# Kernel optimization log

Measured on AMD Instinct MI355X. Metric: run time of the kernel, lower is better.

## Reference

```python
import jax, jax.numpy as jnp
import numpy as np

D_MODEL = 2048
HQ = 32          # query heads
HKV = 8          # kv heads
HD = D_MODEL // HQ   # head_dim = 64
G = HQ // HKV        # group size = 4
THETA = 10000.0


def _rope(x, pos):
    """x: (B, H, T, D), pos: (B, T) int. Rotates even/odd interleaved pairs."""
    D = x.shape[-1]
    inv_freq = THETA ** (-jnp.arange(0, D, 2, dtype=jnp.float32) / D)   # (D/2,)
    ang = pos[:, None, :, None].astype(jnp.float32) * inv_freq          # (B,1,T,D/2)
    cos, sin = jnp.cos(ang), jnp.sin(ang)
    x1, x2 = x[..., 0::2], x[..., 1::2]
    r1 = x1 * cos - x2 * sin
    r2 = x1 * sin + x2 * cos
    return jnp.stack([r1, r2], axis=-1).reshape(x.shape)


def setup_inputs() -> dict:
    key = jax.random.key(0)
    ks = jax.random.split(key, 5)
    B, T = 2, 2048
    s = lambda fan_in: 1.0 / np.sqrt(fan_in)
    return {
        "x": jax.random.normal(ks[0], (B, T, D_MODEL), jnp.float32),
        "token_positions": jnp.arange(T, dtype=jnp.int32),
        "WQ": jax.random.normal(ks[1], (HQ * HD, D_MODEL), jnp.float32) * s(D_MODEL),
        "WK": jax.random.normal(ks[2], (HKV * HD, D_MODEL), jnp.float32) * s(D_MODEL),
        "WV": jax.random.normal(ks[3], (HKV * HD, D_MODEL), jnp.float32) * s(D_MODEL),
        "WO": jax.random.normal(ks[4], (D_MODEL, HQ * HD), jnp.float32) * s(HQ * HD),
    }


def reference(x, token_positions, WQ, WK, WV, WO):
    B, T, _ = x.shape
    pos = token_positions if token_positions.ndim == 2 else jnp.broadcast_to(token_positions[None, :], (B, T))

    # Projections (Linear is y = x @ W.T, no bias)
    Q = (x @ WQ.T).reshape(B, T, HQ, HD).transpose(0, 2, 1, 3)    # (B,Hq,T,D)
    K = (x @ WK.T).reshape(B, T, HKV, HD).transpose(0, 2, 1, 3)   # (B,Hkv,T,D)
    V = (x @ WV.T).reshape(B, T, HKV, HD).transpose(0, 2, 1, 3)

    Q = _rope(Q, pos)
    K = _rope(K, pos)

    # GQA: group query heads per kv head instead of duplicating K/V
    Qg = Q.reshape(B, HKV, G, T, HD)
    scale = jnp.float32(1.0 / np.sqrt(HD))
    scores = jnp.einsum('bkgqd,bkld->bkgql', Qg, K) * scale       # (B,Hkv,G,T,T)

    causal = jnp.tril(jnp.ones((T, T), dtype=bool))
    scores = jnp.where(causal, scores, jnp.finfo(scores.dtype).min)
    A = jax.nn.softmax(scores, axis=-1)

    O = jnp.einsum('bkgql,bkld->bkgqd', A, V)                     # (B,Hkv,G,T,D)
    O = O.reshape(B, HQ, T, HD).transpose(0, 2, 1, 3).reshape(B, T, HQ * HD)
    return O @ WO.T
```

## Files before the change

### kernel.cpp

```cpp
#include <hip/hip_runtime.h>
#include <hip/hip_bf16.h>

#define B_   2
#define T_   2048
#define DM_  2048
#define HQ_  32
#define HKV_ 8
#define HD_  64

typedef __attribute__((ext_vector_type(8))) short bf16x8;
typedef __attribute__((ext_vector_type(4))) float f32x4;
typedef __fp16 f16x4 __attribute__((ext_vector_type(4)));
typedef __fp16 f16x2 __attribute__((ext_vector_type(2)));

__device__ __forceinline__ unsigned short f2bf(float f) {
    unsigned int u = __float_as_uint(f);
    u = (u + 0x7fffu + ((u >> 16) & 1u)) >> 16;
    return (unsigned short)u;
}

__device__ __forceinline__ void gload16(const unsigned short* g, unsigned short* l) {
    __builtin_amdgcn_global_load_lds(
        (const __attribute__((address_space(1))) unsigned int*)g,
        (__attribute__((address_space(3))) unsigned int*)l, 16, 0, 0);
}


__global__ __launch_bounds__(256) void convert_all(
    const float* __restrict__ x,  const float* __restrict__ WQ,
    const float* __restrict__ WK, const float* __restrict__ WV,
    const float* __restrict__ WO, unsigned short* __restrict__ ws)
{
    int i = blockIdx.x*256 + threadIdx.x;
    const float* src; unsigned short* dst; int rel;
    if (i < 2097152)      { src = x;  dst = ws;                 rel = i; }
    else if (i < 3145728) { src = WQ; dst = ws + 8388608;       rel = i - 2097152; }
    else if (i < 3407872) { src = WK; dst = ws + 8388608+4194304; rel = i - 3145728; }
    else if (i < 3670016) { src = WV; dst = ws + 8388608+5242880; rel = i - 3407872; }
    else                  { src = WO; dst = ws + 14680064;      rel = i - 3670016; }
    float4 v = *(const float4*)(src + (size_t)rel*4);
    uint2 pk;
    pk.x = (unsigned int)f2bf(v.x) | ((unsigned int)f2bf(v.y) << 16);
    pk.y = (unsigned int)f2bf(v.z) | ((unsigned int)f2bf(v.w) << 16);
    *(uint2*)(dst + (size_t)rel*4) = pk;
}

__global__ __launch_bounds__(256) void qkv_gemm_bf16(
    const unsigned short* __restrict__ Ab, const unsigned short* __restrict__ Wb,
    unsigned short* __restrict__ Qb, unsigned short* __restrict__ Kb,
    unsigned short* __restrict__ Vt)
{
    __shared__ unsigned short As[128*32];
    __shared__ unsigned short Bs[128*32];
    const int tid  = threadIdx.x;
    const int ln   = tid & 63;
    const int wv   = tid >> 6;
    const int wm   = (wv >> 1) * 64;
    const int wn   = (wv & 1) * 64;
    const int col  = ln & 15;
    const int quad = ln >> 4;
    const int m0   = blockIdx.y * 128;
    const int n0   = blockIdx.x * 128;

    const unsigned short* aG = Ab + (size_t)(m0 + (tid>>2))*DM_ + (tid&3)*8;
    const unsigned short* bG = Wb + (size_t)(n0 + (tid>>2))*DM_ + (tid&3)*8;
    unsigned short* aL0 = &As[wv*512];
    unsigned short* aL1 = &As[wv*512 + 2048];
    unsigned short* bL0 = &Bs[wv*512];
    unsigned short* bL1 = &Bs[wv*512 + 2048];

    f32x4 acc[4][4];
    #pragma unroll
    for (int i=0;i<4;++i)
        #pragma unroll
        for (int j=0;j<4;++j) { acc[i][j][0]=0.f; acc[i][j][1]=0.f; acc[i][j][2]=0.f; acc[i][j][3]=0.f; }

    for (int k0 = 0; k0 < DM_; k0 += 32) {
        __syncthreads();
        gload16(aG + k0,                  aL0);
        gload16(aG + (size_t)64*DM_ + k0, aL1);
        gload16(bG + k0,                  bL0);
        gload16(bG + (size_t)64*DM_ + k0, bL1);
        __syncthreads();
        bf16x8 af[4], bfr[4];
        #pragma unroll
        for (int i=0;i<4;++i) {
            af[i]  = *(const bf16x8*)&As[(wm + i*16 + col)*32 + quad*8];
            bfr[i] = *(const bf16x8*)&Bs[(wn + i*16 + col)*32 + quad*8];
        }
        #pragma unroll
        for (int i=0;i<4;++i)
            #pragma unroll
            for (int j=0;j<4;++j)
                acc[i][j] = __builtin_amdgcn_mfma_f32_16x16x32_bf16(af[i], bfr[j], acc[i][j], 0, 0, 0);
    }

    const int b  = m0 >> 11;
    const int tb = m0 & 2047;
    #pragma unroll
    for (int j=0;j<4;++j) {
        const int n = n0 + wn + j*16 + col;
        #pragma unroll
        for (int i=0;i<4;++i) {
            const int t = tb + wm + i*16 + quad*4;
            if (n < 2048) {
                #pragma unroll
                for (int r=0;r<4;++r)
                    Qb[(((size_t)(b*HQ_ + (n>>6)))*T_ + t + r)*HD_ + (n&63)] = f2bf(acc[i][j][r]);
            } else if (n < 2560) {
                #pragma unroll
                for (int r=0;r<4;++r)
                    Kb[(((size_t)(b*HKV_ + ((n-2048)>>6)))*T_ + t + r)*HD_ + (n&63)] = f2bf(acc[i][j][r]);
            } else {
                unsigned short* vp = Vt + (((size_t)(b*HKV_ + ((n-2560)>>6)))*HD_ + (n&63))*T_ + t;
                union { f16x2 h; unsigned int u; } c0, c1;
                c0.h = __builtin_amdgcn_cvt_pkrtz(acc[i][j][0], acc[i][j][1]);
                c1.h = __builtin_amdgcn_cvt_pkrtz(acc[i][j][2], acc[i][j][3]);
                *(unsigned int*)(vp)     = c0.u;
                *(unsigned int*)(vp + 2) = c1.u;
            }
        }
    }
}

__global__ __launch_bounds__(256) void rope_inplace(
    unsigned short* __restrict__ Qb, unsigned short* __restrict__ Kb,
    const int* __restrict__ pos)
{
    const int NQ = B_*HQ_*T_*(HD_/2);
    const int NK = B_*HKV_*T_*(HD_/2);
    int idx = blockIdx.x*256 + threadIdx.x;
    unsigned short* base; float scale;
    int rem;
    if (idx < NQ) { base = Qb; rem = idx; scale = 0.18033688011112042f; }
    else { rem = idx - NQ; if (rem >= NK) return; base = Kb; scale = 1.0f; }
    const int i  = rem & 31;
    const int t  = (rem >> 5) & (T_ - 1);
    const int bh = rem >> 16;
    size_t off = (((size_t)bh)*T_ + t)*HD_ + (i<<1);
    unsigned int pk = *(unsigned int*)(base + off);
    float x1 = __uint_as_float((pk & 0xffffu) << 16);
    float x2 = __uint_as_float(pk & 0xffff0000u);
    float p = (float)pos[t];
    float inv = exp2f(-13.287712379549449f * ((float)(i<<1)) * (1.0f/64.0f));
    float ang = p * inv;
    float sn, cs;
    sincosf(ang, &sn, &cs);
    float r1 = (x1*cs - x2*sn) * scale;
    float r2 = (x1*sn + x2*cs) * scale;
    unsigned int out = (unsigned int)f2bf(r1) | ((unsigned int)f2bf(r2) << 16);
    *(unsigned int*)(base + off) = out;
}

__global__ __launch_bounds__(256, 2) void attn_mfma(
    const unsigned short* __restrict__ Qb, const unsigned short* __restrict__ Kb,
    const unsigned short* __restrict__ Vh, unsigned short* __restrict__ Ob)
{
    __shared__ unsigned short Ks[2][64*64];
    __shared__ unsigned short Vs[2][64*64];

    const int tid  = threadIdx.x;
    const int lane = tid & 63;
    const int wave = tid >> 6;
    const int q16  = lane & 15;
    const int quad = lane >> 4;
    const int bxi  = blockIdx.x;
    const int bh   = blockIdx.y;
    const int b    = bh >> 5;
    const int h    = bh & 31;
    const int kvh  = h >> 2;
    const int qa   = bxi;
    const int qbt  = 31 - bxi;
    const int qgA  = qa *64 + wave*16 + q16;
    const int qgB  = qbt*64 + wave*16 + q16;

    const unsigned short* kbase = Kb + ((size_t)(b*HKV_ + kvh))*T_*HD_;
    const unsigned short* vbase = Vh + ((size_t)(b*HKV_ + kvh))*(size_t)HD_*T_;

    const bf16x8 qA0 = *(const bf16x8*)(Qb + ((size_t)bh*T_ + qgA)*HD_ + quad*8);
    const bf16x8 qA1 = *(const bf16x8*)(Qb + ((size_t)bh*T_ + qgA)*HD_ + 32 + quad*8);
    const bf16x8 qB0 = *(const bf16x8*)(Qb + ((size_t)bh*T_ + qgB)*HD_ + quad*8);
    const bf16x8 qB1 = *(const bf16x8*)(Qb + ((size_t)bh*T_ + qgB)*HD_ + 32 + quad*8);

    f32x4 oA[4], oB[4];
    #pragma unroll
    for (int i=0;i<4;++i) {
        oA[i][0]=0.f; oA[i][1]=0.f; oA[i][2]=0.f; oA[i][3]=0.f;
        oB[i][0]=0.f; oB[i][1]=0.f; oB[i][2]=0.f; oB[i][3]=0.f;
    }
    float lA = 0.f, lB = 0.f;

    const int sr = tid >> 3;
    const int sj = tid & 7;
    const int sc = (sj ^ (sr & 7)) * 8;

    const int rk7 = q16 & 7;
    const int ck0 = (quad ^ rk7) * 8;
    const int ck1 = ((quad + 4) ^ rk7) * 8;

    auto smrow = [&](const f32x4 s, float& ps) -> f16x4 {
        float e0 = exp2f(s[0]), e1 = exp2f(s[1]);
        float e2 = exp2f(s[2]), e3 = exp2f(s[3]);
        ps += (e0+e1) + (e2+e3);
        union { f16x2 h[2]; f16x4 v; } c;
        c.h[0] = __builtin_amdgcn_cvt_pkrtz(e0, e1);
        c.h[1] = __builtin_amdgcn_cvt_pkrtz(e2, e3);
        return c.v;
    };

    uint4 kr0, kr1, vr0, vr1;
    kr0 = *(const uint4*)(kbase + (size_t)sr*HD_ + sj*8);
    kr1 = *(const uint4*)(kbase + (size_t)(sr+32)*HD_ + sj*8);
    vr0 = *(const uint4*)(vbase + (size_t)sr*T_ + sj*8);
    vr1 = *(const uint4*)(vbase + (size_t)(sr+32)*T_ + sj*8);
    *(uint4*)&Ks[0][sr*64 + sc]      = kr0;
    *(uint4*)&Ks[0][(sr+32)*64 + sc] = kr1;
    *(uint4*)&Vs[0][sr*64 + sc]      = vr0;
    *(uint4*)&Vs[0][(sr+32)*64 + sc] = vr1;
    kr0 = *(const uint4*)(kbase + (size_t)(64+sr)*HD_ + sj*8);
    kr1 = *(const uint4*)(kbase + (size_t)(64+sr+32)*HD_ + sj*8);
    vr0 = *(const uint4*)(vbase + (size_t)sr*T_ + 64 + sj*8);
    vr1 = *(const uint4*)(vbase + (size_t)(sr+32)*T_ + 64 + sj*8);
    __syncthreads();

    int cur = 0;

    for (int kt = 0; kt <= qa; ++kt) {
        const unsigned short* KsC = Ks[cur];
        const unsigned short* VsC = Vs[cur];
        const int nxt = cur ^ 1;

        f32x4 sB[4], sA[4];
        #pragma unroll
        for (int t=0;t<4;++t) {
            sB[t][0]=0.f; sB[t][1]=0.f; sB[t][2]=0.f; sB[t][3]=0.f;
            sA[t][0]=0.f; sA[t][1]=0.f; sA[t][2]=0.f; sA[t][3]=0.f;
        }
        f16x4 pfB[4];
        float psB = 0.f, psA = 0.f;

        __builtin_amdgcn_s_setprio(1);
        #pragma unroll
        for (int t = 0; t < 4; ++t) {
            const int rk = (t*16 + q16) * 64;
            bf16x8 a0 = *(const bf16x8*)&KsC[rk + ck0];
            bf16x8 a1 = *(const bf16x8*)&KsC[rk + ck1];
            sB[t] = __builtin_amdgcn_mfma_f32_16x16x32_bf16(a0, qB0, sB[t], 0, 0, 0);
            sB[t] = __builtin_amdgcn_mfma_f32_16x16x32_bf16(a1, qB1, sB[t], 0, 0, 0);
            sA[t] = __builtin_amdgcn_mfma_f32_16x16x32_bf16(a0, qA0, sA[t], 0, 0, 0);
            sA[t] = __builtin_amdgcn_mfma_f32_16x16x32_bf16(a1, qA1, sA[t], 0, 0, 0);
            if (t > 0) pfB[t-1] = smrow(sB[t-1], psB);
        }
        *(uint4*)&Ks[nxt][sr*64 + sc]      = kr0;
        *(uint4*)&Ks[nxt][(sr+32)*64 + sc] = kr1;
        *(uint4*)&Vs[nxt][sr*64 + sc]      = vr0;
        *(uint4*)&Vs[nxt][(sr+32)*64 + sc] = vr1;
        if (kt + 1 < qbt) {
            const int kn = (kt+2)*64;
            kr0 = *(const uint4*)(kbase + (size_t)(kn+sr)*HD_ + sj*8);
            kr1 = *(const uint4*)(kbase + (size_t)(kn+sr+32)*HD_ + sj*8);
            vr0 = *(const uint4*)(vbase + (size_t)sr*T_ + kn + sj*8);
            vr1 = *(const uint4*)(vbase + (size_t)(sr+32)*T_ + kn + sj*8);
        }
        pfB[3] = smrow(sB[3], psB);
        lB += psB;

        if (kt == qa) {
            #pragma unroll
            for (int t = 0; t < 4; ++t)
                #pragma unroll
                for (int r = 0; r < 4; ++r)
                    if (kt*64 + t*16 + quad*4 + r > qgA) sA[t][r] = -1e30f;
        }

        #pragma unroll
        for (int t = 0; t < 4; ++t) {
            const int cv = ((2*t + (quad>>1)) ^ rk7) * 8 + (quad&1)*4;
            f16x4 va[4];
            #pragma unroll
            for (int dt=0;dt<4;++dt)
                va[dt] = *(const f16x4*)&VsC[(dt*16 + q16)*64 + cv];
            #pragma unroll
            for (int dt=0;dt<4;++dt)
                oB[dt] = __builtin_amdgcn_mfma_f32_16x16x16f16(va[dt], pfB[t], oB[dt], 0, 0, 0);
            f16x4 pfA = smrow(sA[t], psA);
            #pragma unroll
            for (int dt=0;dt<4;++dt)
                oA[dt] = __builtin_amdgcn_mfma_f32_16x16x16f16(va[dt], pfA, oA[dt], 0, 0, 0);
        }
        lA += psA;
        __builtin_amdgcn_s_setprio(0);
        __syncthreads();
        cur ^= 1;
    }

    for (int kt = qa+1; kt <= qbt; ++kt) {
        const unsigned short* KsC = Ks[cur];
        const unsigned short* VsC = Vs[cur];
        const int nxt = cur ^ 1;

        f32x4 sB[4];
        #pragma unroll
        for (int t=0;t<4;++t) { sB[t][0]=0.f; sB[t][1]=0.f; sB[t][2]=0.f; sB[t][3]=0.f; }

        __builtin_amdgcn_s_setprio(1);
        #pragma unroll
        for (int t = 0; t < 4; ++t) {
            const int rk = (t*16 + q16) * 64;
            bf16x8 a0 = *(const bf16x8*)&KsC[rk + ck0];
            bf16x8 a1 = *(const bf16x8*)&KsC[rk + ck1];
            sB[t] = __builtin_amdgcn_mfma_f32_16x16x32_bf16(a0, qB0, sB[t], 0, 0, 0);
            sB[t] = __builtin_amdgcn_mfma_f32_16x16x32_bf16(a1, qB1, sB[t], 0, 0, 0);
        }
        if (kt < qbt) {
            *(uint4*)&Ks[nxt][sr*64 + sc]      = kr0;
            *(uint4*)&Ks[nxt][(sr+32)*64 + sc] = kr1;
            *(uint4*)&Vs[nxt][sr*64 + sc]      = vr0;
            *(uint4*)&Vs[nxt][(sr+32)*64 + sc] = vr1;
        }
        if (kt + 1 < qbt) {
            const int kn = (kt+2)*64;
            kr0 = *(const uint4*)(kbase + (size_t)(kn+sr)*HD_ + sj*8);
            kr1 = *(const uint4*)(kbase + (size_t)(kn+sr+32)*HD_ + sj*8);
            vr0 = *(const uint4*)(vbase + (size_t)sr*T_ + kn + sj*8);
            vr1 = *(const uint4*)(vbase + (size_t)(sr+32)*T_ + kn + sj*8);
        }
        if (kt == qbt) {
            #pragma unroll
            for (int t = 0; t < 4; ++t)
                #pragma unroll
                for (int r = 0; r < 4; ++r)
                    if (kt*64 + t*16 + quad*4 + r > qgB) sB[t][r] = -1e30f;
        }

        float psB = 0.f;
        #pragma unroll
        for (int t = 0; t < 4; ++t) {
            f16x4 pfB = smrow(sB[t], psB);
            const int cv = ((2*t + (quad>>1)) ^ rk7) * 8 + (quad&1)*4;
            #pragma unroll
            for (int dt=0;dt<4;++dt) {
                f16x4 va = *(const f16x4*)&VsC[(dt*16 + q16)*64 + cv];
                oB[dt] = __builtin_amdgcn_mfma_f32_16x16x16f16(va, pfB, oB[dt], 0, 0, 0);
            }
        }
        lB += psB;
        __builtin_amdgcn_s_setprio(0);
        __syncthreads();
        cur ^= 1;
    }

    lA += __shfl_xor(lA, 16); lA += __shfl_xor(lA, 32);
    lB += __shfl_xor(lB, 16); lB += __shfl_xor(lB, 32);
    const float rlA = 1.0f / lA;
    const float rlB = 1.0f / lB;
    unsigned short* opA = Ob + ((size_t)(b*T_ + qgA))*(HQ_*HD_) + h*HD_;
    unsigned short* opB = Ob + ((size_t)(b*T_ + qgB))*(HQ_*HD_) + h*HD_;
    #pragma unroll
    for (int dt = 0; dt < 4; ++dt) {
        uint2 pa, pb;
        pa.x = (unsigned int)f2bf(oA[dt][0]*rlA) | ((unsigned int)f2bf(oA[dt][1]*rlA) << 16);
        pa.y = (unsigned int)f2bf(oA[dt][2]*rlA) | ((unsigned int)f2bf(oA[dt][3]*rlA) << 16);
        pb.x = (unsigned int)f2bf(oB[dt][0]*rlB) | ((unsigned int)f2bf(oB[dt][1]*rlB) << 16);
        pb.y = (unsigned int)f2bf(oB[dt][2]*rlB) | ((unsigned int)f2bf(oB[dt][3]*rlB) << 16);
        *(uint2*)(opA + dt*16 + quad*4) = pa;
        *(uint2*)(opB + dt*16 + quad*4) = pb;
    }
}

__global__ __launch_bounds__(256) void out_gemm_bf16(
    const unsigned short* __restrict__ Ab, const unsigned short* __restrict__ Wb,
    float* __restrict__ C)
{
    __shared__ unsigned short As[128*32];
    __shared__ unsigned short Bs[128*32];
    const int tid  = threadIdx.x;
    const int ln   = tid & 63;
    const int wv   = tid >> 6;
    const int wm   = (wv >> 1) * 64;
    const int wn   = (wv & 1) * 64;
    const int col  = ln & 15;
    const int quad = ln >> 4;
    const int m0   = blockIdx.y * 128;
    const int n0   = blockIdx.x * 128;

    const unsigned short* aG = Ab + (size_t)(m0 + (tid>>2))*DM_ + (tid&3)*8;
    const unsigned short* bG = Wb + (size_t)(n0 + (tid>>2))*DM_ + (tid&3)*8;
    unsigned short* aL0 = &As[wv*512];
    unsigned short* aL1 = &As[wv*512 + 2048];
    unsigned short* bL0 = &Bs[wv*512];
    unsigned short* bL1 = &Bs[wv*512 + 2048];

    f32x4 acc[4][4];
    #pragma unroll
    for (int i=0;i<4;++i)
        #pragma unroll
        for (int j=0;j<4;++j) { acc[i][j][0]=0.f; acc[i][j][1]=0.f; acc[i][j][2]=0.f; acc[i][j][3]=0.f; }

    for (int k0 = 0; k0 < DM_; k0 += 32) {
        __syncthreads();
        gload16(aG + k0,                  aL0);
        gload16(aG + (size_t)64*DM_ + k0, aL1);
        gload16(bG + k0,                  bL0);
        gload16(bG + (size_t)64*DM_ + k0, bL1);
        __syncthreads();
        bf16x8 af[4], bfr[4];
        #pragma unroll
        for (int i=0;i<4;++i) {
            af[i]  = *(const bf16x8*)&As[(wm + i*16 + col)*32 + quad*8];
            bfr[i] = *(const bf16x8*)&Bs[(wn + i*16 + col)*32 + quad*8];
        }
        #pragma unroll
        for (int i=0;i<4;++i)
            #pragma unroll
            for (int j=0;j<4;++j)
                acc[i][j] = __builtin_amdgcn_mfma_f32_16x16x32_bf16(af[i], bfr[j], acc[i][j], 0, 0, 0);
    }

    #pragma unroll
    for (int i=0;i<4;++i) {
        const int m = m0 + wm + i*16 + quad*4;
        #pragma unroll
        for (int j=0;j<4;++j) {
            const int n = n0 + wn + j*16 + col;
            #pragma unroll
            for (int r=0;r<4;++r)
                C[(size_t)(m + r)*DM_ + n] = acc[i][j][r];
        }
    }
}

extern "C" void kernel_launch(void* const* d_in, const int* in_sizes, int n_in,
                              void* d_out, int out_size, void* d_ws, size_t ws_size,
                              hipStream_t stream) {
    const float* x   = (const float*)d_in[0];
    const int*   pos = (const int*)  d_in[1];
    const float* WQ  = (const float*)d_in[2];
    const float* WK  = (const float*)d_in[3];
    const float* WV  = (const float*)d_in[4];
    const float* WO  = (const float*)d_in[5];
    float* out = (float*)d_out;

    unsigned short* xb  = (unsigned short*)d_ws;
    unsigned short* Wb  = xb  + (size_t)8388608;
    unsigned short* WOb = Wb  + (size_t)6291456;
    unsigned short* Qb  = WOb + (size_t)4194304;
    unsigned short* Kb  = Qb  + (size_t)8388608;
    unsigned short* Vt  = Kb  + (size_t)2097152;
    unsigned short* Ob  = Vt  + (size_t)2097152;

    convert_all<<<18432, 256, 0, stream>>>(x, WQ, WK, WV, WO, (unsigned short*)d_ws);

    dim3 g1(24, 32);
    qkv_gemm_bf16<<<g1, 256, 0, stream>>>(xb, Wb, Qb, Kb, Vt);

    const int pairs = B_*HQ_*T_*(HD_/2) + B_*HKV_*T_*(HD_/2);
    rope_inplace<<<(pairs + 255)/256, 256, 0, stream>>>(Qb, Kb, pos);

    dim3 g3(16, B_*HQ_);
    attn_mfma<<<g3, 256, 0, stream>>>(Qb, Kb, Vt, Ob);

    dim3 g4(16, 32);
    out_gemm_bf16<<<g4, 256, 0, stream>>>(Ob, WOb, out);
}
```

Before: 337.7 us.

## Double-buffer LDS tiles and XOR-swizzle layout in projection GEMMs

The QKV and output projection GEMMs now use two LDS buffers. The next K-tile is loaded with global_load_lds while the MFMAs run on the current tile, and there is one barrier per iteration instead of two. The 16-byte chunk placement within each LDS row is XOR-swizzled so that the fragment reads spread across banks and avoid conflicts. This doubles LDS use per block and relies on the async load having completed by the time the following barrier is reached.

Result: no change. 335.3 us (-0.7%).

```diff
diff --git a/kernel.cpp b/kernel.cpp
--- a/kernel.cpp
+++ b/kernel.cpp
@@ -50,8 +50,8 @@
     unsigned short* __restrict__ Qb, unsigned short* __restrict__ Kb,
     unsigned short* __restrict__ Vt)
 {
-    __shared__ unsigned short As[128*32];
-    __shared__ unsigned short Bs[128*32];
+    __shared__ unsigned short As[2][128*32];
+    __shared__ unsigned short Bs[2][128*32];
     const int tid  = threadIdx.x;
     const int ln   = tid & 63;
     const int wv   = tid >> 6;
@@ -62,12 +62,10 @@
     const int m0   = blockIdx.y * 128;
     const int n0   = blockIdx.x * 128;
 
-    const unsigned short* aG = Ab + (size_t)(m0 + (tid>>2))*DM_ + (tid&3)*8;
-    const unsigned short* bG = Wb + (size_t)(n0 + (tid>>2))*DM_ + (tid&3)*8;
-    unsigned short* aL0 = &As[wv*512];
-    unsigned short* aL1 = &As[wv*512 + 2048];
-    unsigned short* bL0 = &Bs[wv*512];
-    unsigned short* bL1 = &Bs[wv*512 + 2048];
+    const int cg = ((tid & 3) ^ ((tid >> 3) & 3)) * 8;
+    const unsigned short* aG = Ab + (size_t)(m0 + (tid>>2))*DM_ + cg;
+    const unsigned short* bG = Wb + (size_t)(n0 + (tid>>2))*DM_ + cg;
+    const int ck = (quad ^ ((col >> 1) & 3)) * 8;
 
     f32x4 acc[4][4];
     #pragma unroll
@@ -75,24 +73,39 @@
         #pragma unroll
         for (int j=0;j<4;++j) { acc[i][j][0]=0.f; acc[i][j][1]=0.f; acc[i][j][2]=0.f; acc[i][j][3]=0.f; }
 
+    {
+        unsigned short* aL = &As[0][wv*512];
+        unsigned short* bL = &Bs[0][wv*512];
+        gload16(aG,                  aL);
+        gload16(aG + (size_t)64*DM_, aL + 2048);
+        gload16(bG,                  bL);
+        gload16(bG + (size_t)64*DM_, bL + 2048);
+    }
+    __syncthreads();
+
+    int cur = 0;
     for (int k0 = 0; k0 < DM_; k0 += 32) {
-        __syncthreads();
-        gload16(aG + k0,                  aL0);
-        gload16(aG + (size_t)64*DM_ + k0, aL1);
-        gload16(bG + k0,                  bL0);
-        gload16(bG + (size_t)64*DM_ + k0, bL1);
-        __syncthreads();
+        if (k0 + 32 < DM_) {
+            unsigned short* aL = &As[cur^1][wv*512];
+            unsigned short* bL = &Bs[cur^1][wv*512];
+            gload16(aG + k0 + 32,                  aL);
+            gload16(aG + (size_t)64*DM_ + k0 + 32, aL + 2048);
+            gload16(bG + k0 + 32,                  bL);
+            gload16(bG + (size_t)64*DM_ + k0 + 32, bL + 2048);
+        }
         bf16x8 af[4], bfr[4];
         #pragma unroll
         for (int i=0;i<4;++i) {
-            af[i]  = *(const bf16x8*)&As[(wm + i*16 + col)*32 + quad*8];
-            bfr[i] = *(const bf16x8*)&Bs[(wn + i*16 + col)*32 + quad*8];
+            af[i]  = *(const bf16x8*)&As[cur][(wm + i*16 + col)*32 + ck];
+            bfr[i] = *(const bf16x8*)&Bs[cur][(wn + i*16 + col)*32 + ck];
         }
         #pragma unroll
         for (int i=0;i<4;++i)
             #pragma unroll
             for (int j=0;j<4;++j)
                 acc[i][j] = __builtin_amdgcn_mfma_f32_16x16x32_bf16(af[i], bfr[j], acc[i][j], 0, 0, 0);
+        __syncthreads();
+        cur ^= 1;
     }
 
     const int b  = m0 >> 11;
@@ -372,8 +385,8 @@
     const unsigned short* __restrict__ Ab, const unsigned short* __restrict__ Wb,
     float* __restrict__ C)
 {
-    __shared__ unsigned short As[128*32];
-    __shared__ unsigned short Bs[128*32];
+    __shared__ unsigned short As[2][128*32];
+    __shared__ unsigned short Bs[2][128*32];
     const int tid  = threadIdx.x;
     const int ln   = tid & 63;
     const int wv   = tid >> 6;
@@ -384,12 +397,10 @@
     const int m0   = blockIdx.y * 128;
     const int n0   = blockIdx.x * 128;
 
-    const unsigned short* aG = Ab + (size_t)(m0 + (tid>>2))*DM_ + (tid&3)*8;
-    const unsigned short* bG = Wb + (size_t)(n0 + (tid>>2))*DM_ + (tid&3)*8;
-    unsigned short* aL0 = &As[wv*512];
-    unsigned short* aL1 = &As[wv*512 + 2048];
-    unsigned short* bL0 = &Bs[wv*512];
-    unsigned short* bL1 = &Bs[wv*512 + 2048];
+    const int cg = ((tid & 3) ^ ((tid >> 3) & 3)) * 8;
+    const unsigned short* aG = Ab + (size_t)(m0 + (tid>>2))*DM_ + cg;
+    const unsigned short* bG = Wb + (size_t)(n0 + (tid>>2))*DM_ + cg;
+    const int ck = (quad ^ ((col >> 1) & 3)) * 8;
 
     f32x4 acc[4][4];
     #pragma unroll
@@ -397,24 +408,39 @@
         #pragma unroll
         for (int j=0;j<4;++j) { acc[i][j][0]=0.f; acc[i][j][1]=0.f; acc[i][j][2]=0.f; acc[i][j][3]=0.f; }
 
+    {
+        unsigned short* aL = &As[0][wv*512];
+        unsigned short* bL = &Bs[0][wv*512];
+        gload16(aG,                  aL);
+        gload16(aG + (size_t)64*DM_, aL + 2048);
+        gload16(bG,                  bL);
+        gload16(bG + (size_t)64*DM_, bL + 2048);
+    }
+    __syncthreads();
+
+    int cur = 0;
     for (int k0 = 0; k0 < DM_; k0 += 32) {
-        __syncthreads();
-        gload16(aG + k0,                  aL0);
-        gload16(aG + (size_t)64*DM_ + k0, aL1);
-        gload16(bG + k0,                  bL0);
-        gload16(bG + (size_t)64*DM_ + k0, bL1);
-        __syncthreads();
+        if (k0 + 32 < DM_) {
+            unsigned short* aL = &As[cur^1][wv*512];
+            unsigned short* bL = &Bs[cur^1][wv*512];
+            gload16(aG + k0 + 32,                  aL);
+            gload16(aG + (size_t)64*DM_ + k0 + 32, aL + 2048);
+            gload16(bG + k0 + 32,                  bL);
+            gload16(bG + (size_t)64*DM_ + k0 + 32, bL + 2048);
+        }
         bf16x8 af[4], bfr[4];
         #pragma unroll
         for (int i=0;i<4;++i) {
-            af[i]  = *(const bf16x8*)&As[(wm + i*16 + col)*32 + quad*8];
-            bfr[i] = *(const bf16x8*)&Bs[(wn + i*16 + col)*32 + quad*8];
+            af[i]  = *(const bf16x8*)&As[cur][(wm + i*16 + col)*32 + ck];
+            bfr[i] = *(const bf16x8*)&Bs[cur][(wn + i*16 + col)*32 + ck];
         }
         #pragma unroll
         for (int i=0;i<4;++i)
             #pragma unroll
             for (int j=0;j<4;++j)
                 acc[i][j] = __builtin_amdgcn_mfma_f32_16x16x32_bf16(af[i], bfr[j], acc[i][j], 0, 0, 0);
+        __syncthreads();
+        cur ^= 1;
     }
 
     #pragma unroll
```
